# Kernel optimization log

Hardware: AMD Instinct MI355X
Metric: run time of the kernel (lower is better)

The kernel has to match this reference:

```python
import jax, jax.numpy as jnp
import numpy as np

HEADS = 8
DIM_HEAD = 64
TOP_K = 1024
KMEANS_ITERS = 4  # the original KMeans class is external; we use Lloyd's algorithm, init = first TOP_K points


def chan_ln(x, g, b):
    # ChanLayerNorm3D: normalize over channel dim (axis=1), biased variance
    m = x.mean(axis=1, keepdims=True)
    v = x.var(axis=1, keepdims=True)
    return g.reshape(1, -1, 1, 1, 1) * (x - m) / (jnp.sqrt(v) + 1e-6) + b.reshape(1, -1, 1, 1, 1)


def kmeans_fit(x, k, iters):
    # x: [N, d] -> centroids [k, d]
    cent0 = x[:k]

    def step(_, cent):
        d2 = (x * x).sum(-1, keepdims=True) - 2.0 * (x @ cent.T) + (cent * cent).sum(-1)
        assign = jnp.argmin(d2, axis=-1)
        sums = jax.ops.segment_sum(x, assign, num_segments=k)
        cnt = jax.ops.segment_sum(jnp.ones((x.shape[0],), x.dtype), assign, num_segments=k)
        new = sums / jnp.maximum(cnt, 1.0)[:, None]
        return jnp.where(cnt[:, None] > 0, new, cent)  # keep old centroid for empty clusters

    return jax.lax.fori_loop(0, iters, step, cent0)


def select_best_idx(q, k, top_k):
    # q: [B, i, d], k: [B, j, d] -> indices [B, top_k] of keys farthest (L1) from their assigned q-centroid
    B, j, d = k.shape
    qf = q.reshape(-1, d)
    kf = k.reshape(-1, d)
    cent = kmeans_fit(qf, top_k, KMEANS_ITERS)
    d2 = (kf * kf).sum(-1, keepdims=True) - 2.0 * (kf @ cent.T) + (cent * cent).sum(-1)
    kc = jnp.argmin(d2, axis=-1)  # predict cluster of each key
    centers = cent[kc].reshape(B, j, d)
    dist = jnp.abs(centers - k).sum(-1)  # [B, j], L1 distance to assigned centroid
    return jnp.argsort(-dist, axis=1)[:, :top_k]


def dpca(query_source, context, w_q, w_kv, w_out, cn_g, cn_b, qn_g, qn_b, on_g, on_b, gamma):
    b, c, D, H, W = query_source.shape
    ctx = chan_ln(context, cn_g, cn_b)
    qs = chan_ln(query_source, qn_g, qn_b)
    # 1x1x1 convs == per-voxel channel matmuls
    kv = jnp.einsum('oc,bcdhw->bodhw', w_kv, ctx)
    k3, v3 = jnp.split(kv, 2, axis=1)
    q3 = jnp.einsum('oc,bcdhw->bodhw', w_q, qs)

    def fold_flat(t, norm):
        bb = t.shape[0]
        t = t.reshape(bb * HEADS, DIM_HEAD, *t.shape[2:])  # fold heads into batch
        if norm:  # F.normalize over channel dim, eps=1e-12
            t = t / jnp.maximum(jnp.linalg.norm(t, axis=1, keepdims=True), 1e-12)
        return t.reshape(bb * HEADS, DIM_HEAD, -1).transpose(0, 2, 1)  # [B, tokens, d]

    q = fold_flat(q3, True)
    k = fold_flat(k3, True)
    v = fold_flat(v3, False)

    idx = select_best_idx(jax.lax.stop_gradient(q), jax.lax.stop_gradient(k), TOP_K)
    k = jnp.take_along_axis(k, idx[:, :, None], axis=1)
    v = jnp.take_along_axis(v, idx[:, :, None], axis=1)

    attn = jax.nn.softmax(jnp.einsum('bid,bjd->bij', q, k), axis=-1)
    out = jnp.einsum('bij,bjd->bid', attn, v)
    out = out.reshape(b, HEADS, D, H, W, DIM_HEAD).transpose(0, 1, 5, 2, 3, 4)
    out = out.reshape(b, HEADS * DIM_HEAD, D, H, W)
    out = jnp.einsum('oc,bcdhw->bodhw', w_out, out)
    out = chan_ln(out, on_g, on_b)
    return gamma * out + query_source


def setup_inputs() -> dict:
    key = jax.random.key(0)
    ks = jax.random.split(key, 6)
    dim, inner, b = 256, HEADS * DIM_HEAD, 2
    query_source = jax.random.normal(ks[0], (b, dim, 16, 16, 16), jnp.float32)
    context = jax.random.normal(ks[1], (b, dim, 8, 16, 16), jnp.float32)
    s_in = 1.0 / np.sqrt(dim)
    return {
        'query_source': query_source,
        'context': context,
        'w_q': jax.random.normal(ks[2], (inner, dim), jnp.float32) * s_in,
        'w_kv': jax.random.normal(ks[3], (2 * inner, dim), jnp.float32) * s_in,
        'w_out': jax.random.normal(ks[4], (dim, inner), jnp.float32) * (1.0 / np.sqrt(inner)),
        'cn_g': jnp.ones((dim,), jnp.float32), 'cn_b': jnp.zeros((dim,), jnp.float32),
        'qn_g': jnp.ones((dim,), jnp.float32), 'qn_b': jnp.zeros((dim,), jnp.float32),
        'on_g': jnp.ones((dim,), jnp.float32), 'on_b': jnp.zeros((dim,), jnp.float32),
        'gamma': jnp.full((1,), 0.5, jnp.float32),  # torch inits to 0 (trivial output); 0.5 makes the test meaningful
    }


def reference(query_source, context, w_q, w_kv, w_out, cn_g, cn_b, qn_g, qn_b, on_g, on_b, gamma):
    return dpca(query_source, context, w_q, w_kv, w_out, cn_g, cn_b, qn_g, qn_b, on_g, on_b, gamma)
```

## Files before the change

### kernel.cpp

```cpp
#include <hip/hip_runtime.h>
#include <math.h>

#define BB 2
#define CDIM 256
#define NQ 4096
#define NK 2048
#define BH 16
#define TOPK 1024
#define NPQ (BH*NQ)
#define NPK (BH*NK)

typedef __attribute__((ext_vector_type(8))) short bfx8;
typedef __attribute__((ext_vector_type(8))) _Float16 hfx8;
typedef __attribute__((ext_vector_type(2))) __fp16 fpx2;
typedef __attribute__((ext_vector_type(4))) float fx4;
typedef __attribute__((ext_vector_type(4))) unsigned short us4;

__device__ inline unsigned short f2bf(float x) {
  unsigned u = __float_as_uint(x);
  return (unsigned short)((u + 0x7fffu + ((u >> 16) & 1u)) >> 16);
}
__device__ inline unsigned short f2h_bits(float x) {
  _Float16 h = (_Float16)x;
  unsigned short u;
  __builtin_memcpy(&u, &h, 2);
  return u;
}
__device__ inline float h_bits2f(unsigned short u) {
  _Float16 h;
  __builtin_memcpy(&h, &u, 2);
  return (float)h;
}

__global__ __launch_bounds__(256) void chan_ln_tsplit_k(
    const float* __restrict__ x, const float* __restrict__ g,
    const float* __restrict__ bta, unsigned short* __restrict__ yh,
    unsigned short* __restrict__ yl, int C, int N) {
  __shared__ float tile[4][64][65];
  __shared__ float p1[4][64], p2[4][64];
  __shared__ float mArr[64], invArr[64];
  int t = threadIdx.x, lane = t & 63, wv = t >> 6;
  int n0 = blockIdx.x * 64, bi = blockIdx.y;
  const float* xb = x + (size_t)bi * C * N + n0 + lane;
  float s = 0.f, s2 = 0.f;
  for (int cl = 0; cl < 64; ++cl) {
    float v = xb[(size_t)(wv * 64 + cl) * N];
    tile[wv][cl][lane] = v;
    s += v;
    s2 += v * v;
  }
  p1[wv][lane] = s;
  p2[wv][lane] = s2;
  __syncthreads();
  if (t < 64) {
    float ts = p1[0][t] + p1[1][t] + p1[2][t] + p1[3][t];
    float ts2 = p2[0][t] + p2[1][t] + p2[2][t] + p2[3][t];
    float m = ts / C;
    float var = ts2 / C - m * m;
    mArr[t] = m;
    invArr[t] = 1.f / (sqrtf(fmaxf(var, 0.f)) + 1e-6f);
  }
  __syncthreads();
  int c = wv * 64 + lane;
  float gc = g[c], bc = bta[c];
  unsigned short* ohb = yh + ((size_t)bi * N + n0) * C + c;
  unsigned short* olb = yl + ((size_t)bi * N + n0) * C + c;
  for (int pl = 0; pl < 64; ++pl) {
    float v = tile[wv][lane][pl];
    float ln = gc * (v - mArr[pl]) * invArr[pl] + bc;
    unsigned short hb = f2h_bits(ln);
    ohb[(size_t)pl * C] = hb;
    olb[(size_t)pl * C] = f2h_bits((ln - h_bits2f(hb)) * 2048.f);
  }
}

__global__ __launch_bounds__(256) void gemm_mfma_k(
    const float* __restrict__ W, const unsigned short* __restrict__ Xh,
    const unsigned short* __restrict__ Xl, float* __restrict__ Y,
    int O, int C, int N) {
  int t = threadIdx.x, lane = t & 63, wv = t >> 6;
  int lq = lane & 15, lg = lane >> 4;
  int n0 = blockIdx.x * 64, o0 = blockIdx.y * 64 + wv * 16;
  int b = blockIdx.z;
  const unsigned short* xbh = Xh + ((size_t)b * N + n0) * C;
  const unsigned short* xbl = Xl + ((size_t)b * N + n0) * C;
  const float* wr = W + (size_t)(o0 + lq) * C;
  fx4 ahi[4], alo[4];
  for (int nt = 0; nt < 4; ++nt) {
    ahi[nt] = (fx4){0.f, 0.f, 0.f, 0.f};
    alo[nt] = (fx4){0.f, 0.f, 0.f, 0.f};
  }
  for (int k0 = 0; k0 < C; k0 += 32) {
    float4 w0 = *(const float4*)(wr + k0 + lg * 8);
    float4 w1 = *(const float4*)(wr + k0 + lg * 8 + 4);
    float wv8[8] = {w0.x, w0.y, w0.z, w0.w, w1.x, w1.y, w1.z, w1.w};
    hfx8 ah, al;
#pragma unroll
    for (int i = 0; i < 8; ++i) {
      _Float16 h = (_Float16)wv8[i];
      ah[i] = h;
      al[i] = (_Float16)((wv8[i] - (float)h) * 2048.f);
    }
#pragma unroll
    for (int nt = 0; nt < 4; ++nt) {
      const unsigned short* bph = xbh + (size_t)(nt * 16 + lq) * C + k0 + lg * 8;
      const unsigned short* bpl = xbl + (size_t)(nt * 16 + lq) * C + k0 + lg * 8;
      hfx8 bh = *(const hfx8*)bph;
      hfx8 bl = *(const hfx8*)bpl;
      ahi[nt] = __builtin_amdgcn_mfma_f32_16x16x32_f16(ah, bh, ahi[nt], 0, 0, 0);
      alo[nt] = __builtin_amdgcn_mfma_f32_16x16x32_f16(al, bh, alo[nt], 0, 0, 0);
      alo[nt] = __builtin_amdgcn_mfma_f32_16x16x32_f16(ah, bl, alo[nt], 0, 0, 0);
    }
  }
  float* yb = Y + ((size_t)b * O + o0) * N + n0;
#pragma unroll
  for (int nt = 0; nt < 4; ++nt)
#pragma unroll
    for (int r = 0; r < 4; ++r)
      yb[(size_t)(lg * 4 + r) * N + nt * 16 + lq] = ahi[nt][r] + alo[nt][r] * (1.f / 2048.f);
}

template <int PATH>
__global__ __launch_bounds__(256) void gemmfold_k(
    const float* __restrict__ W, const unsigned short* __restrict__ Xh,
    const unsigned short* __restrict__ Xl, float* __restrict__ fq,
    unsigned short* __restrict__ sh, unsigned short* __restrict__ sl,
    unsigned short* __restrict__ b16, float* __restrict__ fv,
    int C, int N) {
  __shared__ __align__(16) unsigned short xlds[2][64][64];
  __shared__ float ftile[64][65];
  __shared__ float part[4][64];
  __shared__ float invArr[64];
  int t = threadIdx.x, lane = t & 63, wv = t >> 6;
  int lq = lane & 15, lg = lane >> 4;
  int n0 = blockIdx.x * 64, o0 = blockIdx.y * 64 + wv * 16;
  int b = blockIdx.z;
  bool isV = (PATH == 1) && (blockIdx.y >= 8);
  int h = (PATH == 1) ? (blockIdx.y & 7) : blockIdx.y;
  const unsigned short* xbh = Xh + ((size_t)b * N + n0) * C;
  const unsigned short* xbl = Xl + ((size_t)b * N + n0) * C;
  const float* wr = W + (size_t)(o0 + lq) * C;

  int a = t * 16;
  int srow = a >> 6;
  int schunk = (a >> 4) & 3;
  const unsigned short* gsh = xbh + (size_t)srow * C + schunk * 8;
  const unsigned short* gsl = xbl + (size_t)srow * C + schunk * 8;
  int swz = (srow & 7) << 4;
  int wbh = srow * 128 + ((schunk * 16) ^ swz);
  int wbl = srow * 128 + ((64 + schunk * 16) ^ swz);
  int rswz = (lq & 7) << 4;
  int xh0 = (lg * 16) ^ rswz;
  int xl0 = (64 + lg * 16) ^ rswz;

  fx4 ahi[4], alo[4];
  for (int nt = 0; nt < 4; ++nt) {
    ahi[nt] = (fx4){0.f, 0.f, 0.f, 0.f};
    alo[nt] = (fx4){0.f, 0.f, 0.f, 0.f};
  }

  {
    uint4 h0 = *(const uint4*)(gsh);
    uint4 l0 = *(const uint4*)(gsl);
    *(uint4*)((char*)&xlds[0][0][0] + wbh) = h0;
    *(uint4*)((char*)&xlds[0][0][0] + wbl) = l0;
  }
  float4 w0c = *(const float4*)(wr + lg * 8);
  float4 w1c = *(const float4*)(wr + lg * 8 + 4);

  for (int s = 0; s < 8; ++s) {
    int cur = s & 1;
    __syncthreads();
    uint4 nh, nl;
    float4 nw0, nw1;
    if (s < 7) {
      nh = *(const uint4*)(gsh + (s + 1) * 32);
      nl = *(const uint4*)(gsl + (s + 1) * 32);
      nw0 = *(const float4*)(wr + (s + 1) * 32 + lg * 8);
      nw1 = *(const float4*)(wr + (s + 1) * 32 + lg * 8 + 4);
    }
    __builtin_amdgcn_sched_barrier(0);
    float wv8[8] = {w0c.x, w0c.y, w0c.z, w0c.w, w1c.x, w1c.y, w1c.z, w1c.w};
    hfx8 ah, al;
#pragma unroll
    for (int i = 0; i < 8; ++i) {
      _Float16 hh = (_Float16)wv8[i];
      ah[i] = hh;
      al[i] = (_Float16)((wv8[i] - (float)hh) * 2048.f);
    }
    const char* Xb = (const char*)&xlds[cur][0][0];
#pragma unroll
    for (int nt = 0; nt < 4; ++nt) {
      int rb = (nt * 16 + lq) * 128;
      hfx8 bh = *(const hfx8*)(Xb + rb + xh0);
      hfx8 bl = *(const hfx8*)(Xb + rb + xl0);
      ahi[nt] = __builtin_amdgcn_mfma_f32_16x16x32_f16(ah, bh, ahi[nt], 0, 0, 0);
      alo[nt] = __builtin_amdgcn_mfma_f32_16x16x32_f16(al, bh, alo[nt], 0, 0, 0);
      alo[nt] = __builtin_amdgcn_mfma_f32_16x16x32_f16(ah, bl, alo[nt], 0, 0, 0);
    }
    __builtin_amdgcn_sched_barrier(0);
    if (s < 7) {
      *(uint4*)((char*)&xlds[cur ^ 1][0][0] + wbh) = nh;
      *(uint4*)((char*)&xlds[cur ^ 1][0][0] + wbl) = nl;
      w0c = nw0;
      w1c = nw1;
    }
  }

  float val[4][4];
#pragma unroll
  for (int nt = 0; nt < 4; ++nt)
#pragma unroll
    for (int r = 0; r < 4; ++r)
      val[nt][r] = ahi[nt][r] + alo[nt][r] * (1.f / 2048.f);
  __syncthreads();
  if (!isV) {
#pragma unroll
    for (int nt = 0; nt < 4; ++nt) {
      float ss = val[nt][0] * val[nt][0] + val[nt][1] * val[nt][1] +
                 val[nt][2] * val[nt][2] + val[nt][3] * val[nt][3];
      ss += __shfl_xor(ss, 16);
      ss += __shfl_xor(ss, 32);
      if (lg == 0) part[wv][nt * 16 + lq] = ss;
    }
    __syncthreads();
    if (t < 64) {
      float tot = part[0][t] + part[1][t] + part[2][t] + part[3][t];
      invArr[t] = 1.f / fmaxf(sqrtf(tot), 1e-12f);
    }
    __syncthreads();
#pragma unroll
    for (int nt = 0; nt < 4; ++nt) {
      float iv = invArr[nt * 16 + lq];
#pragma unroll
      for (int r = 0; r < 4; ++r) val[nt][r] *= iv;
    }
    __syncthreads();
  }
#pragma unroll
  for (int nt = 0; nt < 4; ++nt)
#pragma unroll
    for (int r = 0; r < 4; ++r)
      ftile[nt * 16 + lq][wv * 16 + lg * 4 + r] = val[nt][r];
  __syncthreads();
  size_t rowb = (size_t)(b * 8 + h) * N + n0;
  for (int r2 = 0; r2 < 16; ++r2) {
    int n = r2 * 4 + wv;
    float v = ftile[n][lane];
    size_t idx = (rowb + n) * 64 + lane;
    if (PATH == 1 && isV) {
      fv[idx] = v;
    } else {
      fq[idx] = v;
      unsigned short hb = f2h_bits(v);
      sh[idx] = hb;
      sl[idx] = f2h_bits((v - h_bits2f(hb)) * 2048.f);
      if (PATH == 0) b16[idx] = hb;
    }
  }
}

__global__ void centprep_k(const float* __restrict__ cent, float* __restrict__ csq,
                           unsigned short* __restrict__ cb2h, unsigned short* __restrict__ cb2l) {
  int j = blockIdx.x, lane = threadIdx.x;
  float c = cent[j * 64 + lane];
  float s = c * c;
  for (int off = 32; off; off >>= 1) s += __shfl_xor(s, off);
  if (lane == 0) csq[j] = s;
  float m2 = -2.f * c;
  unsigned short h = f2h_bits(m2);
  cb2h[j * 64 + lane] = h;
  cb2l[j * 64 + lane] = f2h_bits((m2 - h_bits2f(h)) * 2048.f);
}

template <int DUO>
__global__ __launch_bounds__(256) void assign_mfma_k(
    const unsigned short* __restrict__ xh, const unsigned short* __restrict__ xl,
    const unsigned short* __restrict__ cb2h, const unsigned short* __restrict__ cb2l,
    const float* __restrict__ csq, int* __restrict__ aout) {
  __shared__ __align__(16) unsigned short clds[2][2][1024];
  int t = threadIdx.x, lane = t & 63, wv = t >> 6;
  int lq = lane & 15, lg = lane >> 4;
  int p0 = blockIdx.x * (DUO ? 128 : 64) + wv * (DUO ? 32 : 16);
  const unsigned short* xbA = xh + (size_t)(p0 + lq) * 64;
  const unsigned short* xlA = xl + (size_t)(p0 + lq) * 64;
  hfx8 ba0 = *(const hfx8*)(xbA + lg * 8);
  hfx8 ba1 = *(const hfx8*)(xbA + 32 + lg * 8);
  hfx8 la0 = *(const hfx8*)(xlA + lg * 8);
  hfx8 la1 = *(const hfx8*)(xlA + 32 + lg * 8);
  hfx8 bb0, bb1, lb0, lb1;
  if (DUO) {
    const unsigned short* xbB = xh + (size_t)(p0 + 16 + lq) * 64;
    const unsigned short* xlB = xl + (size_t)(p0 + 16 + lq) * 64;
    bb0 = *(const hfx8*)(xbB + lg * 8);
    bb1 = *(const hfx8*)(xbB + 32 + lg * 8);
    lb0 = *(const hfx8*)(xlB + lg * 8);
    lb1 = *(const hfx8*)(xlB + 32 + lg * 8);
  }

  int part = t >> 7;
  int abyte = (t & 127) * 16;
  int wbyte = abyte ^ (((abyte >> 7) & 7) << 4);
  const unsigned short* gsrc = (part ? cb2l : cb2h) + (abyte >> 1);
  int rowoff = lq * 128;
  int x0 = (lg * 16) ^ ((lq & 7) << 4);
  int x1 = (64 + lg * 16) ^ ((lq & 7) << 4);

  float bestA = 3.4e38f, bestB = 3.4e38f;
  int jA = 0, jB = 0;

  uint4 r0 = *(const uint4*)(gsrc);
  *(uint4*)((char*)&clds[0][part][0] + wbyte) = r0;

  for (int s = 0; s < 64; ++s) {
    int cur = s & 1;
    __syncthreads();
    uint4 rn;
    if (s < 63) rn = *(const uint4*)(gsrc + (size_t)(s + 1) * 1024);
    __builtin_amdgcn_sched_barrier(0);
    const char* ph = (const char*)&clds[cur][0][0];
    const char* pl = (const char*)&clds[cur][1][0];
    hfx8 ah0 = *(const hfx8*)(ph + rowoff + x0);
    hfx8 ah1 = *(const hfx8*)(ph + rowoff + x1);
    hfx8 al0 = *(const hfx8*)(pl + rowoff + x0);
    hfx8 al1 = *(const hfx8*)(pl + rowoff + x1);
    fx4 cq = *(const fx4*)(csq + s * 16 + lg * 4);
    {
      fx4 chi = cq;
      chi = __builtin_amdgcn_mfma_f32_16x16x32_f16(ah0, ba0, chi, 0, 0, 0);
      chi = __builtin_amdgcn_mfma_f32_16x16x32_f16(ah1, ba1, chi, 0, 0, 0);
      fx4 clo = (fx4){0.f, 0.f, 0.f, 0.f};
      clo = __builtin_amdgcn_mfma_f32_16x16x32_f16(ah0, la0, clo, 0, 0, 0);
      clo = __builtin_amdgcn_mfma_f32_16x16x32_f16(ah1, la1, clo, 0, 0, 0);
      clo = __builtin_amdgcn_mfma_f32_16x16x32_f16(al0, ba0, clo, 0, 0, 0);
      clo = __builtin_amdgcn_mfma_f32_16x16x32_f16(al1, ba1, clo, 0, 0, 0);
#pragma unroll
      for (int r_ = 0; r_ < 4; ++r_) {
        int j_ = s * 16 + lg * 4 + r_;
        float d2_ = chi[r_] + clo[r_] * (1.f / 2048.f);
        if (d2_ < bestA) { bestA = d2_; jA = j_; }
      }
    }
    if (DUO) {
      fx4 chi = cq;
      chi = __builtin_amdgcn_mfma_f32_16x16x32_f16(ah0, bb0, chi, 0, 0, 0);
      chi = __builtin_amdgcn_mfma_f32_16x16x32_f16(ah1, bb1, chi, 0, 0, 0);
      fx4 clo = (fx4){0.f, 0.f, 0.f, 0.f};
      clo = __builtin_amdgcn_mfma_f32_16x16x32_f16(ah0, lb0, clo, 0, 0, 0);
      clo = __builtin_amdgcn_mfma_f32_16x16x32_f16(ah1, lb1, clo, 0, 0, 0);
      clo = __builtin_amdgcn_mfma_f32_16x16x32_f16(al0, bb0, clo, 0, 0, 0);
      clo = __builtin_amdgcn_mfma_f32_16x16x32_f16(al1, bb1, clo, 0, 0, 0);
#pragma unroll
      for (int r_ = 0; r_ < 4; ++r_) {
        int j_ = s * 16 + lg * 4 + r_;
        float d2_ = chi[r_] + clo[r_] * (1.f / 2048.f);
        if (d2_ < bestB) { bestB = d2_; jB = j_; }
      }
    }
    __builtin_amdgcn_sched_barrier(0);
    if (s < 63) *(uint4*)((char*)&clds[cur ^ 1][part][0] + wbyte) = rn;
  }

  {
    float o = __shfl_xor(bestA, 16);
    int oj = __shfl_xor(jA, 16);
    if (o < bestA || (o == bestA && oj < jA)) { bestA = o; jA = oj; }
    o = __shfl_xor(bestA, 32);
    oj = __shfl_xor(jA, 32);
    if (o < bestA || (o == bestA && oj < jA)) { bestA = o; jA = oj; }
  }
  if (DUO) {
    float o = __shfl_xor(bestB, 16);
    int oj = __shfl_xor(jB, 16);
    if (o < bestB || (o == bestB && oj < jB)) { bestB = o; jB = oj; }
    o = __shfl_xor(bestB, 32);
    oj = __shfl_xor(jB, 32);
    if (o < bestB || (o == bestB && oj < jB)) { bestB = o; jB = oj; }
  }
  if (lg == 0) {
    aout[p0 + lq] = jA;
    if (DUO) aout[p0 + 16 + lq] = jB;
  }
}

__global__ void dist_k(const float* __restrict__ x, const float* __restrict__ cent,
                       const int* __restrict__ asg, float* __restrict__ dout) {
  int t = threadIdx.x, lane = t & 63, wv = t >> 6;
  int p = blockIdx.x * 4 + wv;
  int a = asg[p];
  float v = fabsf(cent[(size_t)a * 64 + lane] - x[(size_t)p * 64 + lane]);
  for (int off = 32; off; off >>= 1) v += __shfl_xor(v, off);
  if (lane == 0) dout[p] = v;
}

__global__ void segsum_k(const float* __restrict__ x, const int* __restrict__ asg,
                         float* __restrict__ sums, float* __restrict__ cnt) {
  int t = threadIdx.x, lane = t & 63, wv = t >> 6;
  int p = blockIdx.x * 4 + wv;
  int a = asg[p];
  float v = x[(size_t)p * 64 + lane];
  atomicAdd(&sums[a * 64 + lane], v);
  if (lane == 0) atomicAdd(&cnt[a], 1.0f);
}

__global__ __launch_bounds__(256) void centup_prep_k(
    float* __restrict__ cent, float* __restrict__ sums, float* __restrict__ cnt,
    float* __restrict__ csq, unsigned short* __restrict__ cb2h,
    unsigned short* __restrict__ cb2l) {
  int i = blockIdx.x * 256 + threadIdx.x;
  int j = i >> 6, lane = threadIdx.x & 63;
  float c = cnt[j];
  float oldc = cent[i];
  float newc = (c > 0.f) ? sums[i] / fmaxf(c, 1.f) : oldc;
  cent[i] = newc;
  float s = newc * newc;
  for (int off = 32; off; off >>= 1) s += __shfl_xor(s, off);
  if (lane == 0) csq[j] = s;
  float m2 = -2.f * newc;
  unsigned short h = f2h_bits(m2);
  cb2h[i] = h;
  cb2l[i] = f2h_bits((m2 - h_bits2f(h)) * 2048.f);
  sums[i] = 0.f;
  if (lane == 0) cnt[j] = 0.f;
}

__global__ __launch_bounds__(1024) void topk_k(const float* __restrict__ dist,
                                               int* __restrict__ sel) {
  __shared__ unsigned long long keys[2048];
  int bh = blockIdx.x, t = threadIdx.x;
  for (int i = t; i < 2048; i += 1024) {
    float d = dist[bh * 2048 + i];
    unsigned int db = __float_as_uint(d);
    keys[i] = ((unsigned long long)db << 32) | (unsigned int)(2047 - i);
  }
  __syncthreads();
  for (int k = 2; k <= 2048; k <<= 1) {
    for (int j = k >> 1; j > 0; j >>= 1) {
      for (int i = t; i < 2048; i += 1024) {
        int ixj = i ^ j;
        if (ixj > i) {
          unsigned long long a = keys[i], b = keys[ixj];
          bool up = ((i & k) == 0);
          bool sw = up ? (a < b) : (a > b);
          if (sw) { keys[i] = b; keys[ixj] = a; }
        }
      }
      __syncthreads();
    }
  }
  if (t < 1024) sel[bh * 1024 + t] = 2047 - (int)(keys[t] & 0xffffffffu);
}

__global__ void gatherb_k(const float* __restrict__ kbuf, const float* __restrict__ vbuf,
                          const int* __restrict__ sel, unsigned short* __restrict__ kh,
                          unsigned short* __restrict__ vT) {
  __shared__ unsigned short tile[64][66];
  int t = threadIdx.x, lane = t & 63, wv = t >> 6;
  int bh = blockIdx.y, i0 = blockIdx.x * 64;
  for (int r = 0; r < 16; ++r) {
    int i = r * 4 + wv;
    int src = sel[bh * 1024 + i0 + i];
    float kvv = kbuf[((size_t)bh * 2048 + src) * 64 + lane];
    kh[((size_t)bh * 1024 + i0 + i) * 64 + lane] = f2h_bits(kvv);
    float vv = vbuf[((size_t)bh * 2048 + src) * 64 + lane];
    tile[i][lane] = f2h_bits(vv);
  }
  __syncthreads();
  for (int r = 0; r < 16; ++r) {
    int d = r * 4 + wv;
    vT[((size_t)bh * 64 + d) * 1024 + i0 + lane] = tile[lane][d];
  }
}

__global__ __launch_bounds__(256) void attn_mfma_k(
    const unsigned short* __restrict__ qh, const unsigned short* __restrict__ kh,
    const unsigned short* __restrict__ vT,
    unsigned short* __restrict__ oh, unsigned short* __restrict__ ol) {
  __shared__ __align__(16) unsigned short kvlds[2][2][4096];
  __shared__ __align__(16) unsigned short plds[4][16][72];
  int t = threadIdx.x, lane = t & 63, wv = t >> 6;
  int lq = lane & 15, lg = lane >> 4;
  int id = blockIdx.x;
  int bh = (id & 7) * 2 + ((id >> 3) & 1);
  int q0 = (id >> 4) * 64 + wv * 16;
  const unsigned short* qbase = qh + ((size_t)bh * 4096 + q0 + lq) * 64;
  hfx8 qf0 = *(const hfx8*)(qbase + lg * 8);
  hfx8 qf1 = *(const hfx8*)(qbase + 32 + lg * 8);
  fx4 acc[4];
  for (int nt = 0; nt < 4; ++nt) acc[nt] = (fx4){0.f, 0.f, 0.f, 0.f};
  float lsum = 0.f;
  const unsigned short* kbase = kh + (size_t)bh * 1024 * 64;
  const unsigned short* vbase = vT + (size_t)bh * 64 * 1024;

  int srow = t >> 2;
  int scolb = (t & 3) * 32;
  const char* gK = (const char*)kbase + (size_t)srow * 128 + scolb;
  const char* gV = (const char*)vbase + (size_t)srow * 2048 + scolb;
  int sw_w = (srow & 7) << 4;
  int wb0 = srow * 128 + (scolb ^ sw_w);
  int wb1 = srow * 128 + ((scolb + 16) ^ sw_w);

  {
    uint4 k0 = *(const uint4*)(gK);
    uint4 k1 = *(const uint4*)(gK + 16);
    uint4 v0 = *(const uint4*)(gV);
    uint4 v1 = *(const uint4*)(gV + 16);
    *(uint4*)((char*)&kvlds[0][0][0] + wb0) = k0;
    *(uint4*)((char*)&kvlds[0][0][0] + wb1) = k1;
    *(uint4*)((char*)&kvlds[0][1][0] + wb0) = v0;
    *(uint4*)((char*)&kvlds[0][1][0] + wb1) = v1;
  }

  int swr = (lq & 7) << 4;
  int rc0 = (lg * 16) ^ swr;
  int rc1 = (64 + lg * 16) ^ swr;

  for (int s = 0; s < 16; ++s) {
    int cur = s & 1;
    __syncthreads();
    uint4 nk0, nk1, nv0, nv1;
    if (s < 15) {
      const char* gKn = gK + (size_t)(s + 1) * 8192;
      const char* gVn = gV + (size_t)(s + 1) * 128;
      nk0 = *(const uint4*)(gKn);
      nk1 = *(const uint4*)(gKn + 16);
      nv0 = *(const uint4*)(gVn);
      nv1 = *(const uint4*)(gVn + 16);
    }
    __builtin_amdgcn_sched_barrier(0);
    const char* Kb = (const char*)&kvlds[cur][0][0];
    const char* Vb = (const char*)&kvlds[cur][1][0];
    fx4 sS[4];
#pragma unroll
    for (int mt = 0; mt < 4; ++mt) {
      int rowb = (mt * 16 + lq) * 128;
      hfx8 a0 = *(const hfx8*)(Kb + rowb + rc0);
      hfx8 a1 = *(const hfx8*)(Kb + rowb + rc1);
      fx4 c = (fx4){0.f, 0.f, 0.f, 0.f};
      c = __builtin_amdgcn_mfma_f32_16x16x32_f16(a0, qf0, c, 0, 0, 0);
      c = __builtin_amdgcn_mfma_f32_16x16x32_f16(a1, qf1, c, 0, 0, 0);
      sS[mt] = c;
    }
#pragma unroll
    for (int mt = 0; mt < 4; ++mt) {
      float p0 = __expf(sS[mt].x), p1 = __expf(sS[mt].y);
      float p2 = __expf(sS[mt].z), p3 = __expf(sS[mt].w);
      lsum += (p0 + p1) + (p2 + p3);
      fpx2 c01 = __builtin_amdgcn_cvt_pkrtz(p0, p1);
      fpx2 c23 = __builtin_amdgcn_cvt_pkrtz(p2, p3);
      unsigned u01, u23;
      __builtin_memcpy(&u01, &c01, 4);
      __builtin_memcpy(&u23, &c23, 4);
      uint2 pk = {u01, u23};
      *(uint2*)&plds[wv][lq][mt * 16 + lg * 4] = pk;
    }
    hfx8 pa0 = *(const hfx8*)&plds[wv][lq][lg * 8];
    hfx8 pa1 = *(const hfx8*)&plds[wv][lq][32 + lg * 8];
#pragma unroll
    for (int nt = 0; nt < 4; ++nt) {
      int rowb = (nt * 16 + lq) * 128;
      hfx8 b0 = *(const hfx8*)(Vb + rowb + rc0);
      hfx8 b1 = *(const hfx8*)(Vb + rowb + rc1);
      acc[nt] = __builtin_amdgcn_mfma_f32_16x16x32_f16(pa0, b0, acc[nt], 0, 0, 0);
      acc[nt] = __builtin_amdgcn_mfma_f32_16x16x32_f16(pa1, b1, acc[nt], 0, 0, 0);
    }
    __builtin_amdgcn_sched_barrier(0);
    if (s < 15) {
      char* dK = (char*)&kvlds[cur ^ 1][0][0];
      char* dV = (char*)&kvlds[cur ^ 1][1][0];
      *(uint4*)(dK + wb0) = nk0;
      *(uint4*)(dK + wb1) = nk1;
      *(uint4*)(dV + wb0) = nv0;
      *(uint4*)(dV + wb1) = nv1;
    }
  }
  lsum += __shfl_xor(lsum, 16);
  lsum += __shfl_xor(lsum, 32);
  int bi = bh >> 3, hd = bh & 7;
  for (int r = 0; r < 4; ++r) {
    float inv = 1.f / __shfl(lsum, lg * 4 + r);
    size_t rowb = ((size_t)bi * 4096 + q0 + lg * 4 + r) * 512 + hd * 64;
    for (int nt = 0; nt < 4; ++nt) {
      float val = acc[nt][r] * inv;
      unsigned short hb = f2h_bits(val);
      oh[rowb + nt * 16 + lq] = hb;
      ol[rowb + nt * 16 + lq] = f2h_bits((val - h_bits2f(hb)) * 2048.f);
    }
  }
}

__global__ __launch_bounds__(256) void final_k(
    const float* __restrict__ y, const float* __restrict__ g,
    const float* __restrict__ bta, const float* __restrict__ gamma,
    const float* __restrict__ qs, float* __restrict__ out) {
  __shared__ float p1[4][64], p2[4][64];
  __shared__ float mArr[64], invArr[64];
  int t = threadIdx.x, lane = t & 63, wv = t >> 6;
  int n0 = blockIdx.x * 64, bi = blockIdx.y;
  const float* yb = y + (size_t)bi * CDIM * NQ + n0 + lane;
  float s = 0.f, s2 = 0.f;
  for (int cl = 0; cl < 64; ++cl) {
    float v = yb[(size_t)(wv * 64 + cl) * NQ];
    s += v;
    s2 += v * v;
  }
  p1[wv][lane] = s;
  p2[wv][lane] = s2;
  __syncthreads();
  if (t < 64) {
    float ts = p1[0][t] + p1[1][t] + p1[2][t] + p1[3][t];
    float ts2 = p2[0][t] + p2[1][t] + p2[2][t] + p2[3][t];
    float m = ts / CDIM;
    float var = ts2 / CDIM - m * m;
    mArr[t] = m;
    invArr[t] = 1.f / (sqrtf(fmaxf(var, 0.f)) + 1e-6f);
  }
  __syncthreads();
  float gm = gamma[0];
  float m = mArr[lane], inv = invArr[lane];
  const float* qb = qs + (size_t)bi * CDIM * NQ + n0 + lane;
  float* ob = out + (size_t)bi * CDIM * NQ + n0 + lane;
  for (int cl = 0; cl < 64; ++cl) {
    int c = wv * 64 + cl;
    float v = yb[(size_t)c * NQ];
    float ln = g[c] * (v - m) * inv + bta[c];
    ob[(size_t)c * NQ] = gm * ln + qb[(size_t)c * NQ];
  }
}

extern "C" void kernel_launch(void* const* d_in, const int* in_sizes, int n_in,
                              void* d_out, int out_size, void* d_ws, size_t ws_size,
                              hipStream_t stream) {
  const float* qsrc = (const float*)d_in[0];
  const float* ctx = (const float*)d_in[1];
  const float* w_q = (const float*)d_in[2];
  const float* w_kv = (const float*)d_in[3];
  const float* w_out = (const float*)d_in[4];
  const float* cn_g = (const float*)d_in[5];
  const float* cn_b = (const float*)d_in[6];
  const float* qn_g = (const float*)d_in[7];
  const float* qn_b = (const float*)d_in[8];
  const float* on_g = (const float*)d_in[9];
  const float* on_b = (const float*)d_in[10];
  const float* gamma = (const float*)d_in[11];

  if (ws_size < (size_t)22267904 * 4) return;
  float* ws = (float*)d_ws;
  float* r_ctx = ws;
  float* r_kv = r_ctx + 1048576;
  float* r_qs = r_kv + 4194304;
  float* r_q3 = r_qs + 2097152;
  float* qbuf = r_q3 + 4194304;
  float* kbuf = qbuf + 4194304;
  float* vbuf = kbuf + 2097152;
  float* cent = vbuf + 2097152;
  float* csq = cent + 65536;
  float* sums = csq + 1024;
  float* cnt = sums + 65536;
  int* asg = (int*)(cnt + 1024);
  float* dist = (float*)(asg + 65536);
  int* sel = (int*)(dist + 32768);
  float* kgreg = (float*)(sel + 16384);

  unsigned short* ctxth = (unsigned short*)r_ctx;
  unsigned short* ctxtl = ctxth + (size_t)BB * NK * CDIM;
  unsigned short* qsth = (unsigned short*)r_qs;
  unsigned short* qstl = qsth + (size_t)BB * NQ * CDIM;
  unsigned short* qh = (unsigned short*)kgreg;
  unsigned short* kh = (unsigned short*)r_ctx;
  unsigned short* vT = kh + 1048576;
  unsigned short* qbh = (unsigned short*)r_q3;
  unsigned short* qbl = qbh + (size_t)NPQ * 64;
  unsigned short* kbh = (unsigned short*)r_kv;
  unsigned short* kbl = kbh + (size_t)NPK * 64;
  unsigned short* cb2h = (unsigned short*)r_qs;
  unsigned short* cb2l = cb2h + 65536;
  unsigned short* attnth = (unsigned short*)r_kv;
  unsigned short* attntl = attnth + (size_t)BB * NQ * 512;
  float* ybuf = r_qs;

  chan_ln_tsplit_k<<<dim3(NK / 64, BB), 256, 0, stream>>>(ctx, cn_g, cn_b, ctxth, ctxtl, CDIM, NK);
  chan_ln_tsplit_k<<<dim3(NQ / 64, BB), 256, 0, stream>>>(qsrc, qn_g, qn_b, qsth, qstl, CDIM, NQ);
  gemmfold_k<1><<<dim3(NK / 64, 16, BB), 256, 0, stream>>>(
      w_kv, ctxth, ctxtl, kbuf, kbh, kbl, nullptr, vbuf, CDIM, NK);
  gemmfold_k<0><<<dim3(NQ / 64, 8, BB), 256, 0, stream>>>(
      w_q, qsth, qstl, qbuf, qbh, qbl, qh, nullptr, CDIM, NQ);
  hipMemcpyAsync(cent, qbuf, 65536 * sizeof(float), hipMemcpyDeviceToDevice, stream);
  centprep_k<<<1024, 64, 0, stream>>>(cent, csq, cb2h, cb2l);
  hipMemsetAsync(sums, 0, (65536 + 1024) * sizeof(float), stream);
  for (int it = 0; it < 4; ++it) {
    assign_mfma_k<1><<<NPQ / 128, 256, 0, stream>>>(qbh, qbl, cb2h, cb2l, csq, asg);
    segsum_k<<<NPQ / 4, 256, 0, stream>>>(qbuf, asg, sums, cnt);
    centup_prep_k<<<65536 / 256, 256, 0, stream>>>(cent, sums, cnt, csq, cb2h, cb2l);
  }
  assign_mfma_k<0><<<NPK / 64, 256, 0, stream>>>(kbh, kbl, cb2h, cb2l, csq, asg);
  dist_k<<<NPK / 4, 256, 0, stream>>>(kbuf, cent, asg, dist);
  topk_k<<<BH, 1024, 0, stream>>>(dist, sel);
  gatherb_k<<<dim3(TOPK / 64, BH), 256, 0, stream>>>(kbuf, vbuf, sel, kh, vT);
  attn_mfma_k<<<1024, 256, 0, stream>>>(qh, kh, vT, attnth, attntl);
  gemm_mfma_k<<<dim3(NQ / 64, 256 / 64, BB), 256, 0, stream>>>(w_out, attnth, attntl, ybuf, 256, 512, NQ);
  final_k<<<dim3(NQ / 64, BB), 256, 0, stream>>>(ybuf, on_g, on_b, gamma, qsrc, (float*)d_out);
}
```

Baseline: 535.5 us.

## Stage activation tiles through double-buffered swizzled LDS in split-fp16 GEMM

The MFMA GEMM kernel used to read activation hi/lo fragments straight from global memory, and each of the four waves reloaded the same 64-row tile. It now loads each 32-wide K slice cooperatively into a double-buffered LDS tile with an XOR swizzle to avoid bank conflicts. The next slice's activations and weights are prefetched into registers while the current slice runs MFMAs. This cuts redundant global traffic and hides load latency, at the cost of one barrier per K step and extra LDS.

Result: faster. 515.0 us (-3.8%).

```diff
diff --git a/kernel.cpp b/kernel.cpp
--- a/kernel.cpp
+++ b/kernel.cpp
@@ -78,6 +78,7 @@
     const float* __restrict__ W, const unsigned short* __restrict__ Xh,
     const unsigned short* __restrict__ Xl, float* __restrict__ Y,
     int O, int C, int N) {
+  __shared__ __align__(16) unsigned short xlds[2][64][64];
   int t = threadIdx.x, lane = t & 63, wv = t >> 6;
   int lq = lane & 15, lg = lane >> 4;
   int n0 = blockIdx.x * 64, o0 = blockIdx.y * 64 + wv * 16;
@@ -85,31 +86,71 @@
   const unsigned short* xbh = Xh + ((size_t)b * N + n0) * C;
   const unsigned short* xbl = Xl + ((size_t)b * N + n0) * C;
   const float* wr = W + (size_t)(o0 + lq) * C;
+
+  int a = t * 16;
+  int srow = a >> 6;
+  int schunk = (a >> 4) & 3;
+  const unsigned short* gsh = xbh + (size_t)srow * C + schunk * 8;
+  const unsigned short* gsl = xbl + (size_t)srow * C + schunk * 8;
+  int swz = (srow & 7) << 4;
+  int wbh = srow * 128 + ((schunk * 16) ^ swz);
+  int wbl = srow * 128 + ((64 + schunk * 16) ^ swz);
+  int rswz = (lq & 7) << 4;
+  int xh0 = (lg * 16) ^ rswz;
+  int xl0 = (64 + lg * 16) ^ rswz;
+
   fx4 ahi[4], alo[4];
   for (int nt = 0; nt < 4; ++nt) {
     ahi[nt] = (fx4){0.f, 0.f, 0.f, 0.f};
     alo[nt] = (fx4){0.f, 0.f, 0.f, 0.f};
   }
-  for (int k0 = 0; k0 < C; k0 += 32) {
-    float4 w0 = *(const float4*)(wr + k0 + lg * 8);
-    float4 w1 = *(const float4*)(wr + k0 + lg * 8 + 4);
-    float wv8[8] = {w0.x, w0.y, w0.z, w0.w, w1.x, w1.y, w1.z, w1.w};
+
+  {
+    uint4 h0 = *(const uint4*)(gsh);
+    uint4 l0 = *(const uint4*)(gsl);
+    *(uint4*)((char*)&xlds[0][0][0] + wbh) = h0;
+    *(uint4*)((char*)&xlds[0][0][0] + wbl) = l0;
+  }
+  float4 w0c = *(const float4*)(wr + lg * 8);
+  float4 w1c = *(const float4*)(wr + lg * 8 + 4);
+
+  int nsteps = C / 32;
+  for (int s = 0; s < nsteps; ++s) {
+    int cur = s & 1;
+    __syncthreads();
+    uint4 nh, nl;
+    float4 nw0, nw1;
+    if (s < nsteps - 1) {
+      nh = *(const uint4*)(gsh + (s + 1) * 32);
+      nl = *(const uint4*)(gsl + (s + 1) * 32);
+      nw0 = *(const float4*)(wr + (s + 1) * 32 + lg * 8);
+      nw1 = *(const float4*)(wr + (s + 1) * 32 + lg * 8 + 4);
+    }
+    __builtin_amdgcn_sched_barrier(0);
+    float wv8[8] = {w0c.x, w0c.y, w0c.z, w0c.w, w1c.x, w1c.y, w1c.z, w1c.w};
     hfx8 ah, al;
 #pragma unroll
     for (int i = 0; i < 8; ++i) {
-      _Float16 h = (_Float16)wv8[i];
-      ah[i] = h;
-      al[i] = (_Float16)((wv8[i] - (float)h) * 2048.f);
-    }
+      _Float16 hh = (_Float16)wv8[i];
+      ah[i] = hh;
+      al[i] = (_Float16)((wv8[i] - (float)hh) * 2048.f);
+    }
+    const char* Xb = (const char*)&xlds[cur][0][0];
 #pragma unroll
     for (int nt = 0; nt < 4; ++nt) {
-      const unsigned short* bph = xbh + (size_t)(nt * 16 + lq) * C + k0 + lg * 8;
-      const unsigned short* bpl = xbl + (size_t)(nt * 16 + lq) * C + k0 + lg * 8;
-      hfx8 bh = *(const hfx8*)bph;
-      hfx8 bl = *(const hfx8*)bpl;
+      int rb = (nt * 16 + lq) * 128;
+      hfx8 bh = *(const hfx8*)(Xb + rb + xh0);
+      hfx8 bl = *(const hfx8*)(Xb + rb + xl0);
       ahi[nt] = __builtin_amdgcn_mfma_f32_16x16x32_f16(ah, bh, ahi[nt], 0, 0, 0);
       alo[nt] = __builtin_amdgcn_mfma_f32_16x16x32_f16(al, bh, alo[nt], 0, 0, 0);
       alo[nt] = __builtin_amdgcn_mfma_f32_16x16x32_f16(ah, bl, alo[nt], 0, 0, 0);
+    }
+    __builtin_amdgcn_sched_barrier(0);
+    if (s < nsteps - 1) {
+      *(uint4*)((char*)&xlds[cur ^ 1][0][0] + wbh) = nh;
+      *(uint4*)((char*)&xlds[cur ^ 1][0][0] + wbl) = nl;
+      w0c = nw0;
+      w1c = nw1;
     }
   }
   float* yb = Y + ((size_t)b * O + o0) * N + n0;
```
